# Performance work log

Hardware: AMD Instinct MI355X
Metric: run time of the kernel (lower is better)

Reference implementation:

```python
import jax, jax.numpy as jnp
import numpy as np

EPS = 1e-09  # from module __init__ eps


def setup_inputs() -> dict:
    key = jax.random.key(0)
    k1, k2 = jax.random.split(key)
    N = 384 * 384
    input1 = jax.random.normal(k1, (1, 32, 384, 384), dtype=jnp.float32)
    input2 = jax.random.randint(k2, (N, 48), 0, N, dtype=jnp.int64)
    return {"input1": input1, "input2": input2}


def reference(input1, input2):
    # input1: [*, a, b, c] -> UU: [N, a] with N = b*c (pixels), a = features
    a, b, c = input1.shape[1], input1.shape[2], input1.shape[3]
    UU = input1.reshape(a, b * c).T  # [N, a]
    J = input2.shape[0]
    nbr = UU[input2]                      # [J, K, a] gather of neighbor features
    diff = UU[:J][:, None, :] - nbr       # [J, K, a]
    msd = jnp.mean(diff * diff, axis=-1)  # [J, K] mean squared distance
    D = -jnp.sqrt(msd + EPS)              # [J, K]
    W = jax.nn.softmax(D, axis=1)         # softmax over K neighbors
    return W
```

## Files before the change

### kernel.cpp

```cpp
#include <hip/hip_runtime.h>
#include <hip/hip_fp16.h>


#define EPS 1e-9f

typedef _Float16 h2 __attribute__((ext_vector_type(2)));
union V16 { uint4 u; h2 h[4]; };

__global__ __launch_bounds__(256) void transpose_half_kernel(
    const float* __restrict__ in, _Float16* __restrict__ UU, int N) {
  const int p = blockIdx.x * 256 + threadIdx.x;
  if (p >= N) return;
  __half h[32];
#pragma unroll
  for (int f = 0; f < 32; ++f) h[f] = __float2half_rn(in[(size_t)f * N + p]);
  uint4* dst = (uint4*)(UU + (size_t)p * 32);
#pragma unroll
  for (int r = 0; r < 4; ++r) {
    __half2 a = __halves2half2(h[8 * r + 0], h[8 * r + 1]);
    __half2 b = __halves2half2(h[8 * r + 2], h[8 * r + 3]);
    __half2 c = __halves2half2(h[8 * r + 4], h[8 * r + 5]);
    __half2 d = __halves2half2(h[8 * r + 6], h[8 * r + 7]);
    dst[r] = make_uint4(*(unsigned*)&a, *(unsigned*)&b, *(unsigned*)&c, *(unsigned*)&d);
  }
}

__device__ __forceinline__ float dot2acc(h2 d, float s) {
#if __has_builtin(__builtin_amdgcn_fdot2)
  return __builtin_amdgcn_fdot2(d, d, s, false);
#else
  float x = (float)d.x, y = (float)d.y;
  return s + x * x + y * y;
#endif
}

__global__ __launch_bounds__(256) void dist_softmax_kernel(
    const _Float16* __restrict__ UU, const int* __restrict__ idx,
    float* __restrict__ out, int J) {
  const int wave = blockIdx.x * 4 + (threadIdx.x >> 6);
  const int lane = threadIdx.x & 63;
  if (wave >= J) return;
  const int quad = lane >> 2;
  const int q = lane & 3;

  V16 a;
  a.u = *(const uint4*)(UU + (size_t)wave * 32 + q * 8);

  const int* ij = idx + (size_t)wave * 48;
  const int n0 = ij[quad];
  const int n1 = ij[16 + quad];
  const int n2 = ij[32 + quad];

  V16 b0, b1, b2;
  b0.u = *(const uint4*)(UU + (size_t)n0 * 32 + q * 8);
  b1.u = *(const uint4*)(UU + (size_t)n1 * 32 + q * 8);
  b2.u = *(const uint4*)(UU + (size_t)n2 * 32 + q * 8);

  float s0 = 0.f, s1 = 0.f, s2 = 0.f;
#pragma unroll
  for (int i = 0; i < 4; ++i) {
    const h2 av = a.h[i];
    h2 d0 = av - b0.h[i];
    h2 d1 = av - b1.h[i];
    h2 d2 = av - b2.h[i];
    s0 = dot2acc(d0, s0);
    s1 = dot2acc(d1, s1);
    s2 = dot2acc(d2, s2);
  }
  s0 += __shfl_xor(s0, 1); s0 += __shfl_xor(s0, 2);
  s1 += __shfl_xor(s1, 1); s1 += __shfl_xor(s1, 2);
  s2 += __shfl_xor(s2, 1); s2 += __shfl_xor(s2, 2);

  const float D0 = -sqrtf(s0 * (1.0f / 32.0f) + EPS);
  const float D1 = -sqrtf(s1 * (1.0f / 32.0f) + EPS);
  const float D2 = -sqrtf(s2 * (1.0f / 32.0f) + EPS);

  float m = fmaxf(D0, fmaxf(D1, D2));
#pragma unroll
  for (int off = 4; off < 64; off <<= 1) m = fmaxf(m, __shfl_xor(m, off));
  const float e0 = __expf(D0 - m);
  const float e1 = __expf(D1 - m);
  const float e2 = __expf(D2 - m);
  float t = e0 + e1 + e2;
#pragma unroll
  for (int off = 4; off < 64; off <<= 1) t += __shfl_xor(t, off);
  const float inv = 1.0f / t;

  if (q == 0) {
    float* oj = out + (size_t)wave * 48;
    oj[quad] = e0 * inv;
    oj[16 + quad] = e1 * inv;
    oj[32 + quad] = e2 * inv;
  }
}

extern "C" void kernel_launch(void* const* d_in, const int* in_sizes, int n_in,
                              void* d_out, int out_size, void* d_ws, size_t ws_size,
                              hipStream_t stream) {
  const float* in1 = (const float*)d_in[0];
  const int* idx = (const int*)d_in[1];
  float* out = (float*)d_out;
  _Float16* UU = (_Float16*)d_ws;

  const int N = in_sizes[0] / 32;
  const int J = in_sizes[1] / 48;

  transpose_half_kernel<<<(N + 255) / 256, 256, 0, stream>>>(in1, UU, N);

  dist_softmax_kernel<<<(J + 3) / 4, 256, 0, stream>>>(UU, idx, out, J);
}
```

Measured before the change: 163.8 us.

## Process two query rows per wave and drop softmax max-subtraction

```diff
diff --git a/kernel.cpp b/kernel.cpp
--- a/kernel.cpp
+++ b/kernel.cpp
@@ -39,58 +39,73 @@
     float* __restrict__ out, int J) {
   const int wave = blockIdx.x * 4 + (threadIdx.x >> 6);
   const int lane = threadIdx.x & 63;
-  if (wave >= J) return;
+  const int jA = wave * 2;
+  const int jB = jA + 1;
+  if (jA >= J) return;
   const int quad = lane >> 2;
   const int q = lane & 3;
 
-  V16 a;
-  a.u = *(const uint4*)(UU + (size_t)wave * 32 + q * 8);
+  const int* iA = idx + (size_t)jA * 48;
+  const int* iB = idx + (size_t)jB * 48;
+  const int nA0 = iA[quad], nA1 = iA[16 + quad], nA2 = iA[32 + quad];
+  const int nB0 = iB[quad], nB1 = iB[16 + quad], nB2 = iB[32 + quad];
 
-  const int* ij = idx + (size_t)wave * 48;
-  const int n0 = ij[quad];
-  const int n1 = ij[16 + quad];
-  const int n2 = ij[32 + quad];
+  V16 aA, aB, bA0, bA1, bA2, bB0, bB1, bB2;
+  aA.u = *(const uint4*)(UU + (size_t)jA * 32 + q * 8);
+  aB.u = *(const uint4*)(UU + (size_t)jB * 32 + q * 8);
+  bA0.u = *(const uint4*)(UU + (size_t)nA0 * 32 + q * 8);
+  bA1.u = *(const uint4*)(UU + (size_t)nA1 * 32 + q * 8);
+  bA2.u = *(const uint4*)(UU + (size_t)nA2 * 32 + q * 8);
+  bB0.u = *(const uint4*)(UU + (size_t)nB0 * 32 + q * 8);
+  bB1.u = *(const uint4*)(UU + (size_t)nB1 * 32 + q * 8);
+  bB2.u = *(const uint4*)(UU + (size_t)nB2 * 32 + q * 8);
 
-  V16 b0, b1, b2;
-  b0.u = *(const uint4*)(UU + (size_t)n0 * 32 + q * 8);
-  b1.u = *(const uint4*)(UU + (size_t)n1 * 32 + q * 8);
-  b2.u = *(const uint4*)(UU + (size_t)n2 * 32 + q * 8);
-
-  float s0 = 0.f, s1 = 0.f, s2 = 0.f;
+  float sA0 = 0.f, sA1 = 0.f, sA2 = 0.f;
+  float sB0 = 0.f, sB1 = 0.f, sB2 = 0.f;
 #pragma unroll
   for (int i = 0; i < 4; ++i) {
-    const h2 av = a.h[i];
-    h2 d0 = av - b0.h[i];
-    h2 d1 = av - b1.h[i];
-    h2 d2 = av - b2.h[i];
-    s0 = dot2acc(d0, s0);
-    s1 = dot2acc(d1, s1);
-    s2 = dot2acc(d2, s2);
+    const h2 avA = aA.h[i];
+    const h2 avB = aB.h[i];
+    sA0 = dot2acc(avA - bA0.h[i], sA0);
+    sA1 = dot2acc(avA - bA1.h[i], sA1);
+    sA2 = dot2acc(avA - bA2.h[i], sA2);
+    sB0 = dot2acc(avB - bB0.h[i], sB0);
+    sB1 = dot2acc(avB - bB1.h[i], sB1);
+    sB2 = dot2acc(avB - bB2.h[i], sB2);
   }
-  s0 += __shfl_xor(s0, 1); s0 += __shfl_xor(s0, 2);
-  s1 += __shfl_xor(s1, 1); s1 += __shfl_xor(s1, 2);
-  s2 += __shfl_xor(s2, 1); s2 += __shfl_xor(s2, 2);
+  sA0 += __shfl_xor(sA0, 1); sA0 += __shfl_xor(sA0, 2);
+  sA1 += __shfl_xor(sA1, 1); sA1 += __shfl_xor(sA1, 2);
+  sA2 += __shfl_xor(sA2, 1); sA2 += __shfl_xor(sA2, 2);
+  sB0 += __shfl_xor(sB0, 1); sB0 += __shfl_xor(sB0, 2);
+  sB1 += __shfl_xor(sB1, 1); sB1 += __shfl_xor(sB1, 2);
+  sB2 += __shfl_xor(sB2, 1); sB2 += __shfl_xor(sB2, 2);
 
-  const float D0 = -sqrtf(s0 * (1.0f / 32.0f) + EPS);
-  const float D1 = -sqrtf(s1 * (1.0f / 32.0f) + EPS);
-  const float D2 = -sqrtf(s2 * (1.0f / 32.0f) + EPS);
+  const float eA0 = __expf(-sqrtf(sA0 * (1.0f / 32.0f) + EPS));
+  const float eA1 = __expf(-sqrtf(sA1 * (1.0f / 32.0f) + EPS));
+  const float eA2 = __expf(-sqrtf(sA2 * (1.0f / 32.0f) + EPS));
+  const float eB0 = __expf(-sqrtf(sB0 * (1.0f / 32.0f) + EPS));
+  const float eB1 = __expf(-sqrtf(sB1 * (1.0f / 32.0f) + EPS));
+  const float eB2 = __expf(-sqrtf(sB2 * (1.0f / 32.0f) + EPS));
 
-  float m = fmaxf(D0, fmaxf(D1, D2));
+  float tA = eA0 + eA1 + eA2;
+  float tB = eB0 + eB1 + eB2;
 #pragma unroll
-  for (int off = 4; off < 64; off <<= 1) m = fmaxf(m, __shfl_xor(m, off));
-  const float e0 = __expf(D0 - m);
-  const float e1 = __expf(D1 - m);
-  const float e2 = __expf(D2 - m);
-  float t = e0 + e1 + e2;
-#pragma unroll
-  for (int off = 4; off < 64; off <<= 1) t += __shfl_xor(t, off);
-  const float inv = 1.0f / t;
+  for (int off = 4; off < 64; off <<= 1) {
+    tA += __shfl_xor(tA, off);
+    tB += __shfl_xor(tB, off);
+  }
+  const float invA = 1.0f / tA;
+  const float invB = 1.0f / tB;
 
   if (q == 0) {
-    float* oj = out + (size_t)wave * 48;
-    oj[quad] = e0 * inv;
-    oj[16 + quad] = e1 * inv;
-    oj[32 + quad] = e2 * inv;
+    float* oA = out + (size_t)jA * 48;
+    float* oB = out + (size_t)jB * 48;
+    oA[quad] = eA0 * invA;
+    oA[16 + quad] = eA1 * invA;
+    oA[32 + quad] = eA2 * invA;
+    oB[quad] = eB0 * invB;
+    oB[16 + quad] = eB1 * invB;
+    oB[32 + quad] = eB2 * invB;
   }
 }
 
@@ -107,5 +122,5 @@
 
   transpose_half_kernel<<<(N + 255) / 256, 256, 0, stream>>>(in1, UU, N);
 
-  dist_softmax_kernel<<<(J + 3) / 4, 256, 0, stream>>>(UU, idx, out, J);
+  dist_softmax_kernel<<<(J + 7) / 8, 256, 0, stream>>>(UU, idx, out, J);
 }
```

Result: no change. 164.8 us (+0.6%).

## Split feature table into halves and compute distances in two gather passes

Applied to the files above, without the earlier changes.

```diff
diff --git a/kernel.cpp b/kernel.cpp
--- a/kernel.cpp
+++ b/kernel.cpp
@@ -5,23 +5,30 @@
 #define EPS 1e-9f
 
 typedef _Float16 h2 __attribute__((ext_vector_type(2)));
-union V16 { uint4 u; h2 h[4]; };
+union V8 { uint2 u; h2 h[2]; };
 
-__global__ __launch_bounds__(256) void transpose_half_kernel(
-    const float* __restrict__ in, _Float16* __restrict__ UU, int N) {
+__global__ __launch_bounds__(256) void transpose_split_kernel(
+    const float* __restrict__ in, _Float16* __restrict__ A,
+    _Float16* __restrict__ B, int N) {
   const int p = blockIdx.x * 256 + threadIdx.x;
   if (p >= N) return;
   __half h[32];
 #pragma unroll
   for (int f = 0; f < 32; ++f) h[f] = __float2half_rn(in[(size_t)f * N + p]);
-  uint4* dst = (uint4*)(UU + (size_t)p * 32);
+  uint4* dstA = (uint4*)(A + (size_t)p * 16);
+  uint4* dstB = (uint4*)(B + (size_t)p * 16);
 #pragma unroll
-  for (int r = 0; r < 4; ++r) {
+  for (int r = 0; r < 2; ++r) {
     __half2 a = __halves2half2(h[8 * r + 0], h[8 * r + 1]);
     __half2 b = __halves2half2(h[8 * r + 2], h[8 * r + 3]);
     __half2 c = __halves2half2(h[8 * r + 4], h[8 * r + 5]);
     __half2 d = __halves2half2(h[8 * r + 6], h[8 * r + 7]);
-    dst[r] = make_uint4(*(unsigned*)&a, *(unsigned*)&b, *(unsigned*)&c, *(unsigned*)&d);
+    dstA[r] = make_uint4(*(unsigned*)&a, *(unsigned*)&b, *(unsigned*)&c, *(unsigned*)&d);
+    __half2 e = __halves2half2(h[16 + 8 * r + 0], h[16 + 8 * r + 1]);
+    __half2 f_ = __halves2half2(h[16 + 8 * r + 2], h[16 + 8 * r + 3]);
+    __half2 g = __halves2half2(h[16 + 8 * r + 4], h[16 + 8 * r + 5]);
+    __half2 k = __halves2half2(h[16 + 8 * r + 6], h[16 + 8 * r + 7]);
+    dstB[r] = make_uint4(*(unsigned*)&e, *(unsigned*)&f_, *(unsigned*)&g, *(unsigned*)&k);
   }
 }
 
@@ -34,63 +41,96 @@
 #endif
 }
 
-__global__ __launch_bounds__(256) void dist_softmax_kernel(
-    const _Float16* __restrict__ UU, const int* __restrict__ idx,
-    float* __restrict__ out, int J) {
+__global__ __launch_bounds__(256) void pass1_kernel(
+    const _Float16* __restrict__ A, const int* __restrict__ idx,
+    float* __restrict__ partial, int J) {
   const int wave = blockIdx.x * 4 + (threadIdx.x >> 6);
   const int lane = threadIdx.x & 63;
   if (wave >= J) return;
   const int quad = lane >> 2;
   const int q = lane & 3;
 
-  V16 a;
-  a.u = *(const uint4*)(UU + (size_t)wave * 32 + q * 8);
+  const int* ij = idx + (size_t)wave * 48;
+  const int n0 = __builtin_nontemporal_load(ij + quad);
+  const int n1 = __builtin_nontemporal_load(ij + 16 + quad);
+  const int n2 = __builtin_nontemporal_load(ij + 32 + quad);
 
-  const int* ij = idx + (size_t)wave * 48;
-  const int n0 = ij[quad];
-  const int n1 = ij[16 + quad];
-  const int n2 = ij[32 + quad];
-
-  V16 b0, b1, b2;
-  b0.u = *(const uint4*)(UU + (size_t)n0 * 32 + q * 8);
-  b1.u = *(const uint4*)(UU + (size_t)n1 * 32 + q * 8);
-  b2.u = *(const uint4*)(UU + (size_t)n2 * 32 + q * 8);
+  V8 a, b0, b1, b2;
+  a.u = *(const uint2*)(A + (size_t)wave * 16 + q * 4);
+  b0.u = *(const uint2*)(A + (size_t)n0 * 16 + q * 4);
+  b1.u = *(const uint2*)(A + (size_t)n1 * 16 + q * 4);
+  b2.u = *(const uint2*)(A + (size_t)n2 * 16 + q * 4);
 
   float s0 = 0.f, s1 = 0.f, s2 = 0.f;
 #pragma unroll
-  for (int i = 0; i < 4; ++i) {
+  for (int i = 0; i < 2; ++i) {
     const h2 av = a.h[i];
-    h2 d0 = av - b0.h[i];
-    h2 d1 = av - b1.h[i];
-    h2 d2 = av - b2.h[i];
-    s0 = dot2acc(d0, s0);
-    s1 = dot2acc(d1, s1);
-    s2 = dot2acc(d2, s2);
+    s0 = dot2acc(av - b0.h[i], s0);
+    s1 = dot2acc(av - b1.h[i], s1);
+    s2 = dot2acc(av - b2.h[i], s2);
   }
   s0 += __shfl_xor(s0, 1); s0 += __shfl_xor(s0, 2);
   s1 += __shfl_xor(s1, 1); s1 += __shfl_xor(s1, 2);
   s2 += __shfl_xor(s2, 1); s2 += __shfl_xor(s2, 2);
 
-  const float D0 = -sqrtf(s0 * (1.0f / 32.0f) + EPS);
-  const float D1 = -sqrtf(s1 * (1.0f / 32.0f) + EPS);
-  const float D2 = -sqrtf(s2 * (1.0f / 32.0f) + EPS);
+  if (q == 0) {
+    float* oj = partial + (size_t)wave * 48;
+    __builtin_nontemporal_store(s0, oj + quad);
+    __builtin_nontemporal_store(s1, oj + 16 + quad);
+    __builtin_nontemporal_store(s2, oj + 32 + quad);
+  }
+}
 
-  float m = fmaxf(D0, fmaxf(D1, D2));
+__global__ __launch_bounds__(256) void pass2_kernel(
+    const _Float16* __restrict__ B, const int* __restrict__ idx,
+    float* __restrict__ io, int J) {
+  const int wave = blockIdx.x * 4 + (threadIdx.x >> 6);
+  const int lane = threadIdx.x & 63;
+  if (wave >= J) return;
+  const int quad = lane >> 2;
+  const int q = lane & 3;
+
+  const int* ij = idx + (size_t)wave * 48;
+  const int n0 = __builtin_nontemporal_load(ij + quad);
+  const int n1 = __builtin_nontemporal_load(ij + 16 + quad);
+  const int n2 = __builtin_nontemporal_load(ij + 32 + quad);
+
+  V8 a, b0, b1, b2;
+  a.u = *(const uint2*)(B + (size_t)wave * 16 + q * 4);
+  b0.u = *(const uint2*)(B + (size_t)n0 * 16 + q * 4);
+  b1.u = *(const uint2*)(B + (size_t)n1 * 16 + q * 4);
+  b2.u = *(const uint2*)(B + (size_t)n2 * 16 + q * 4);
+
+  float* oj = io + (size_t)wave * 48;
+  const float p0 = __builtin_nontemporal_load(oj + quad);
+  const float p1 = __builtin_nontemporal_load(oj + 16 + quad);
+  const float p2 = __builtin_nontemporal_load(oj + 32 + quad);
+
+  float s0 = 0.f, s1 = 0.f, s2 = 0.f;
 #pragma unroll
-  for (int off = 4; off < 64; off <<= 1) m = fmaxf(m, __shfl_xor(m, off));
-  const float e0 = __expf(D0 - m);
-  const float e1 = __expf(D1 - m);
-  const float e2 = __expf(D2 - m);
+  for (int i = 0; i < 2; ++i) {
+    const h2 av = a.h[i];
+    s0 = dot2acc(av - b0.h[i], s0);
+    s1 = dot2acc(av - b1.h[i], s1);
+    s2 = dot2acc(av - b2.h[i], s2);
+  }
+  s0 += __shfl_xor(s0, 1); s0 += __shfl_xor(s0, 2);
+  s1 += __shfl_xor(s1, 1); s1 += __shfl_xor(s1, 2);
+  s2 += __shfl_xor(s2, 1); s2 += __shfl_xor(s2, 2);
+
+  const float e0 = __expf(-sqrtf((s0 + p0) * (1.0f / 32.0f) + EPS));
+  const float e1 = __expf(-sqrtf((s1 + p1) * (1.0f / 32.0f) + EPS));
+  const float e2 = __expf(-sqrtf((s2 + p2) * (1.0f / 32.0f) + EPS));
+
   float t = e0 + e1 + e2;
 #pragma unroll
   for (int off = 4; off < 64; off <<= 1) t += __shfl_xor(t, off);
   const float inv = 1.0f / t;
 
   if (q == 0) {
-    float* oj = out + (size_t)wave * 48;
-    oj[quad] = e0 * inv;
-    oj[16 + quad] = e1 * inv;
-    oj[32 + quad] = e2 * inv;
+    __builtin_nontemporal_store(e0 * inv, oj + quad);
+    __builtin_nontemporal_store(e1 * inv, oj + 16 + quad);
+    __builtin_nontemporal_store(e2 * inv, oj + 32 + quad);
   }
 }
 
@@ -100,12 +140,15 @@
   const float* in1 = (const float*)d_in[0];
   const int* idx = (const int*)d_in[1];
   float* out = (float*)d_out;
-  _Float16* UU = (_Float16*)d_ws;
 
   const int N = in_sizes[0] / 32;
   const int J = in_sizes[1] / 48;
 
-  transpose_half_kernel<<<(N + 255) / 256, 256, 0, stream>>>(in1, UU, N);
+  _Float16* A = (_Float16*)d_ws;
+  _Float16* B = (_Float16*)d_ws + (size_t)N * 16;
 
-  dist_softmax_kernel<<<(J + 3) / 4, 256, 0, stream>>>(UU, idx, out, J);
+  transpose_split_kernel<<<(N + 255) / 256, 256, 0, stream>>>(in1, A, B, N);
+
+  pass1_kernel<<<(J + 3) / 4, 256, 0, stream>>>(A, idx, out, J);
+  pass2_kernel<<<(J + 3) / 4, 256, 0, stream>>>(B, idx, out, J);
 }
```

After: 204.4 us. 24.7% more time.
